# Performance work log

Measured on AMD Instinct MI355X. Metric: run time of the kernel, lower is better.

The kernel has to match this reference:

```python
import jax, jax.numpy as jnp
import numpy as np

NUM_HEADS = 16
HEAD_DIM = 80  # embed_dim 1280 / 16


def setup_inputs() -> dict:
    key = jax.random.key(0)
    ks = jax.random.split(key, 5)
    E = NUM_HEADS * HEAD_DIM
    sq, b = 1024, 8
    x = jax.random.normal(ks[0], (sq, b, E), dtype=jnp.float32)
    w_in = jax.random.normal(ks[1], (E, 3 * E), dtype=jnp.float32) * (E ** -0.5)
    b_in = jax.random.normal(ks[2], (3 * E,), dtype=jnp.float32) * 0.01
    w_out = jax.random.normal(ks[3], (E, E), dtype=jnp.float32) * (E ** -0.5)
    b_out = jax.random.normal(ks[4], (E,), dtype=jnp.float32) * 0.01
    return {"x": x, "w_in": w_in, "b_in": b_in, "w_out": w_out, "b_out": b_out}


def reference(x, w_in, b_in, w_out, b_out):
    sq, b, E = x.shape
    H, D = NUM_HEADS, HEAD_DIM
    norm_factor = jnp.asarray(D ** 0.5, x.dtype)
    # in_proj: [sq, b, 3E] -> [sq, b, H, 3D], split into q/k/v along last dim
    mixed = (x @ w_in + b_in).reshape(sq, b, H, 3 * D)
    q, k, v = jnp.split(mixed, 3, axis=-1)  # each [sq, b, H, D]
    # merge (b, H) and move to batch-of-bmm layout [b*H, sq, D]
    q = q.reshape(sq, b * H, D).transpose(1, 0, 2) / norm_factor
    k = k.reshape(sq, b * H, D).transpose(1, 0, 2)
    v = v.reshape(sq, b * H, D).transpose(1, 0, 2)
    scores = jnp.einsum('nqd,nkd->nqk', q, k)  # [b*H, sq, sq]
    probs = jax.nn.softmax(scores, axis=-1)
    ctx = jnp.einsum('nqk,nkd->nqd', probs, v)  # [b*H, sq, D]
    # [b, H, sq, D] -> [sq, b, H, D] -> [sq, b, E]
    ctx = ctx.reshape(b, H, sq, D).transpose(2, 0, 1, 3).reshape(sq, b, E)
    return ctx @ w_out + b_out
```

## Files before the change

### kernel.cpp

```cpp
#include <hip/hip_runtime.h>

#define DEVI __device__ __forceinline__

typedef _Float16 f16x8 __attribute__((ext_vector_type(8)));
typedef _Float16 f16x4v __attribute__((ext_vector_type(4)));
typedef _Float16 f16x2 __attribute__((ext_vector_type(2)));
typedef __fp16 fp16x2 __attribute__((ext_vector_type(2)));
typedef float f32x4 __attribute__((ext_vector_type(4)));
typedef float f32x16 __attribute__((ext_vector_type(16)));
typedef unsigned u32x4 __attribute__((ext_vector_type(4)));

DEVI void gl16(const void* g, void* l) {
  __builtin_amdgcn_global_load_lds((const __attribute__((address_space(1))) void*)g,
                                   (__attribute__((address_space(3))) void*)l, 16, 0, 0);
}

#define VMCNT(N) asm volatile("s_waitcnt vmcnt(" #N ")" ::: "memory")
#define LGKM0() asm volatile("s_waitcnt lgkmcnt(0)" ::: "memory")
#define BARRIER() asm volatile("s_barrier" ::: "memory")

DEVI unsigned pk2(float a, float b) {
  fp16x2 t = __builtin_amdgcn_cvt_pkrtz(a, b);
  return __builtin_bit_cast(unsigned, t);
}
DEVI void pl32swap(unsigned &a, unsigned &b) {
  asm volatile("v_permlane32_swap_b32 %0, %1" : "+v"(a), "+v"(b));
}

__global__ __launch_bounds__(256) void k_prep(const float* __restrict__ x, _Float16* __restrict__ xb,
                                              const float* __restrict__ w_in, _Float16* __restrict__ w_inT,
                                              const float* __restrict__ w_out, _Float16* __restrict__ w_outT) {
  __shared__ float t[32][33];
  int bid = blockIdx.x;
  int tid = threadIdx.x;
  if (bid < 2048) {
    const int n4 = 8192 * 1280 / 4;
    for (int i = bid * 256 + tid; i < n4; i += 2048 * 256) {
      float4 v = ((const float4*)x)[i];
      f16x4v h = { (_Float16)v.x, (_Float16)v.y, (_Float16)v.z, (_Float16)v.w };
      ((f16x4v*)xb)[i] = h;
    }
    return;
  }
  const float* in; _Float16* out; int R, C, tIdx; bool perm;
  if (bid < 6848) { in = w_in;  out = w_inT;  R = 1280; C = 3840; tIdx = bid - 2048; perm = true; }
  else            { in = w_out; out = w_outT; R = 1280; C = 1280; tIdx = bid - 6848; perm = false; }
  int ntc = C / 32;
  int cb = (tIdx % ntc) * 32, rb = (tIdx / ntc) * 32;
  int tx = tid & 31, ty = tid >> 5;
  #pragma unroll
  for (int i = ty; i < 32; i += 8) t[i][tx] = in[(size_t)(rb + i) * C + cb + tx];
  __syncthreads();
  #pragma unroll
  for (int i = ty; i < 32; i += 8) {
    int c = cb + i;
    if (perm) {
      int hq = c / 240, tt = c - hq * 240;
      int reg = tt / 80, d = tt - reg * 80;
      c = reg * 1280 + hq * 80 + d;
    }
    out[(size_t)c * R + rb + tx] = (_Float16)t[tx][i];
  }
}


#define MM(NLO, AF, BF) do {                                                                       \
    __builtin_amdgcn_s_setprio(1);                                                                 \
    _Pragma("unroll")                                                                              \
    for (int m_ = 0; m_ < 8; m_++) {                                                               \
      acc[m_][NLO]     = __builtin_amdgcn_mfma_f32_16x16x32_f16(AF[m_], BF[NLO],     acc[m_][NLO],     0, 0, 0); \
      acc[m_][NLO + 1] = __builtin_amdgcn_mfma_f32_16x16x32_f16(AF[m_], BF[NLO + 1], acc[m_][NLO + 1], 0, 0, 0); \
    }                                                                                              \
    __builtin_amdgcn_s_setprio(0);                                                                 \
  } while (0)

#define LDA(KT, KK, DST) do {                                                                      \
    const _Float16* bas_ = &smem[(size_t)((((KT) & 1) * 2) + wr) * 8192];                          \
    _Pragma("unroll")                                                                              \
    for (int m_ = 0; m_ < 8; m_++)                                                                 \
      DST[m_] = *(const f16x8*)&bas_[(m_ * 16 + ln) * 64 + (((((KK) * 4) + g) ^ chB) << 3)];       \
  } while (0)

#define LDB(KT, KK, DST) do {                                                                      \
    const _Float16* bas_ = &smem[32768 + (size_t)((((KT) & 1) * 2) + (wc >> 1)) * 8192];           \
    _Pragma("unroll")                                                                              \
    for (int n_ = 0; n_ < 4; n_++)                                                                 \
      DST[n_] = *(const f16x8*)&bas_[((wc & 1) * 64 + n_ * 16 + ln) * 64 + (((((KK) * 4) + g) ^ chB) << 3)]; \
  } while (0)

template<int M, int N, int K>
__global__ __launch_bounds__(512, 2) void k_gemm8(const _Float16* __restrict__ A, const _Float16* __restrict__ BT,
                                                  const float* __restrict__ bias,
                                                  _Float16* __restrict__ qo, _Float16* __restrict__ ko,
                                                  _Float16* __restrict__ vo) {
  extern __shared__ _Float16 smem[];
  constexpr int NT = K / 64;
  constexpr int NI = NT / 2;
  const int tid = threadIdx.x;
  const int w = tid >> 6, lane = tid & 63, ln = lane & 15, g = lane >> 4;
  const int wr = w >> 2, wc = w & 3;
  const int l8 = lane >> 3, l7 = lane & 7;
  const int stChunk = (l7 ^ l8) << 3;
  const int chB = ln & 7;

  constexpr int MT = M / 256;
  const int xcd = blockIdx.x & 7;
  const int i = blockIdx.x >> 3;
  const int bm0 = (xcd * (MT / 8) + (i & 3)) * 256;
  const int bn0 = (i >> 2) * 256;

  auto stgA = [&](int kt, int hh) {
    _Float16* ldsb = &smem[(size_t)((kt & 1) * 2 + hh) * 8192 + w * 1024];
    const _Float16* g0 = &A[(size_t)(bm0 + hh * 128 + w * 16 + l8) * K + kt * 64 + stChunk];
    gl16(g0, ldsb);
    gl16(g0 + (size_t)8 * K, ldsb + 512);
  };
  auto stgB = [&](int kt, int hh) {
    _Float16* ldsb = &smem[32768 + (size_t)((kt & 1) * 2 + hh) * 8192 + w * 1024];
    const _Float16* g0 = &BT[(size_t)(bn0 + hh * 128 + w * 16 + l8) * K + kt * 64 + stChunk];
    gl16(g0, ldsb);
    gl16(g0 + (size_t)8 * K, ldsb + 512);
  };

  f32x4 acc[8][4] = {};
  f16x8 a0[8], a1[8], b0[4], b1[4];

  stgB(0, 0); stgB(0, 1); stgA(0, 0); stgA(0, 1);
  stgB(1, 0); stgB(1, 1); stgA(1, 0);
  VMCNT(6);
  BARRIER();
  LDA(0, 0, a0); LDB(0, 0, b0);

  for (int it = 0; it < NI; ++it) {
    const int T0 = 2 * it, T1 = 2 * it + 1;
    const int S0 = (T0 + 2 < NT) ? T0 + 2 : 0;
    const int S1 = (T1 + 2 < NT) ? T1 + 2 : 1;
    LDB(T0, 1, b1);
    stgA(T1, 1);
    BARRIER();
    MM(0, a0, b0);
    LGKM0(); BARRIER();
    LDA(T0, 1, a1);
    stgB(S0, 0);
    BARRIER();
    MM(2, a0, b0);
    LGKM0(); BARRIER();
    stgB(S0, 1);
    BARRIER();
    MM(0, a1, b1);
    VMCNT(4);
    LGKM0(); BARRIER();
    LDA(T1, 0, a0); LDB(T1, 0, b0);
    stgA(S0, 0);
    BARRIER();
    MM(2, a1, b1);
    LGKM0(); BARRIER();
    LDB(T1, 1, b1);
    stgA(S0, 1);
    BARRIER();
    MM(0, a0, b0);
    LGKM0(); BARRIER();
    LDA(T1, 1, a1);
    stgB(S1, 0);
    BARRIER();
    MM(2, a0, b0);
    LGKM0(); BARRIER();
    stgB(S1, 1);
    BARRIER();
    MM(0, a1, b1);
    VMCNT(4);
    LGKM0(); BARRIER();
    LDA(S0, 0, a0); LDB(S0, 0, b0);
    stgA(S1, 0);
    BARRIER();
    MM(2, a1, b1);
    LGKM0(); BARRIER();
  }

  VMCNT(0);
  BARRIER();
  _Float16* sH = smem;
  const int regn = bn0 / 1280;
  const int relb = bn0 - regn * 1280;
  #pragma unroll
  for (int n = 0; n < 4; n++) {
    int col = wc * 64 + n * 16 + ln;
    int rel = relb + col;
    int h = rel / 80, d = rel - h * 80;
    float bv = bias[h * 240 + regn * 80 + d];
    float scl = (regn == 0) ? (0.11180339887498948f * 1.4426950408889634f) : 1.0f;
    #pragma unroll
    for (int m = 0; m < 8; m++) {
      #pragma unroll
      for (int r = 0; r < 4; r++) {
        int row = wr * 128 + m * 16 + 4 * g + r;
        sH[row * 256 + col] = (_Float16)((acc[m][n][r] + bv) * scl);
      }
    }
  }
  LGKM0();
  BARRIER();
  _Float16* dst = (regn == 0) ? qo : (regn == 1) ? ko : vo;
  #pragma unroll
  for (int i2 = 0; i2 < 16; i2++) {
    int id = tid + 512 * i2;
    int row = id >> 5, c8 = id & 31;
    f16x8 v = *(const f16x8*)&sH[row * 256 + c8 * 8];
    int rel = relb + c8 * 8;
    int h = rel / 80, d0 = rel - h * 80;
    int grow = bm0 + row;
    *(f16x8*)&dst[(size_t)(((grow & 7) * 16 + h) * 1024 + (grow >> 3)) * 80 + d0] = v;
  }
}


#define MMo(NLO, AF, BF) do {                                                                      \
    __builtin_amdgcn_s_setprio(1);                                                                 \
    _Pragma("unroll")                                                                              \
    for (int m_ = 0; m_ < 4; m_++) {                                                               \
      acc[m_][NLO]     = __builtin_amdgcn_mfma_f32_16x16x32_f16(AF[m_], BF[NLO],     acc[m_][NLO],     0, 0, 0); \
      acc[m_][NLO + 1] = __builtin_amdgcn_mfma_f32_16x16x32_f16(AF[m_], BF[NLO + 1], acc[m_][NLO + 1], 0, 0, 0); \
    }                                                                                              \
    __builtin_amdgcn_s_setprio(0);                                                                 \
  } while (0)

#define LDAo(KT, KK, DST) do {                                                                     \
    const _Float16* bas_ = &smem[(size_t)((KT) & 1) * 8192];                                       \
    _Pragma("unroll")                                                                              \
    for (int m_ = 0; m_ < 4; m_++)                                                                 \
      DST[m_] = *(const f16x8*)&bas_[(wr * 64 + m_ * 16 + ln) * 64 + (((((KK) * 4) + g) ^ chB) << 3)]; \
  } while (0)

#define LDBo(KT, KK, DST) do {                                                                     \
    const _Float16* bas_ = &smem[16384 + (size_t)(((KT) & 1) * 2 + (wc >> 1)) * 8192];             \
    _Pragma("unroll")                                                                              \
    for (int n_ = 0; n_ < 4; n_++)                                                                 \
      DST[n_] = *(const f16x8*)&bas_[((wc & 1) * 64 + n_ * 16 + ln) * 64 + (((((KK) * 4) + g) ^ chB) << 3)]; \
  } while (0)

template<int M, int N, int K>
__global__ __launch_bounds__(512, 2) void k_gemm8o(const _Float16* __restrict__ A, const _Float16* __restrict__ BT,
                                                   const float* __restrict__ bias, float* __restrict__ outF) {
  extern __shared__ _Float16 smem[];
  constexpr int NT = K / 64;
  constexpr int NI = NT / 2;
  const int tid = threadIdx.x;
  const int w = tid >> 6, lane = tid & 63, ln = lane & 15, g = lane >> 4;
  const int wr = w >> 2, wc = w & 3;
  const int l8 = lane >> 3, l7 = lane & 7;
  const int stChunk = (l7 ^ l8) << 3;
  const int chB = ln & 7;

  const int xcd = blockIdx.x & 7;
  const int i = blockIdx.x >> 3;
  const int bm0 = (xcd * 8 + (i & 7)) * 128;
  const int bn0 = (i >> 3) * 256;

  auto stgA = [&](int kt) {
    _Float16* ldsb = &smem[(size_t)(kt & 1) * 8192 + w * 1024];
    const _Float16* g0 = &A[(size_t)(bm0 + w * 16 + l8) * K + kt * 64 + stChunk];
    gl16(g0, ldsb);
    gl16(g0 + (size_t)8 * K, ldsb + 512);
  };
  auto stgB = [&](int kt, int hh) {
    _Float16* ldsb = &smem[16384 + (size_t)((kt & 1) * 2 + hh) * 8192 + w * 1024];
    const _Float16* g0 = &BT[(size_t)(bn0 + hh * 128 + w * 16 + l8) * K + kt * 64 + stChunk];
    gl16(g0, ldsb);
    gl16(g0 + (size_t)8 * K, ldsb + 512);
  };

  f32x4 acc[4][4] = {};
  f16x8 a0[4], a1[4], b0[4], b1[4];

  stgB(0, 0); stgB(0, 1); stgA(0);
  stgB(1, 0); stgB(1, 1); stgA(1);
  VMCNT(6);
  BARRIER();
  LDAo(0, 0, a0); LDBo(0, 0, b0);

  for (int it = 0; it < NI; ++it) {
    const int T0 = 2 * it, T1 = 2 * it + 1;
    const int S0 = (T0 + 2 < NT) ? T0 + 2 : 0;
    const int S1 = (T1 + 2 < NT) ? T1 + 2 : 1;
    LDBo(T0, 1, b1);
    BARRIER(); MMo(0, a0, b0); LGKM0(); BARRIER();
    LDAo(T0, 1, a1);
    stgB(S0, 0);
    BARRIER(); MMo(2, a0, b0); LGKM0(); BARRIER();
    stgB(S0, 1);
    BARRIER(); MMo(0, a1, b1); VMCNT(4); LGKM0(); BARRIER();
    LDAo(T1, 0, a0); LDBo(T1, 0, b0);
    stgA(S0);
    BARRIER(); MMo(2, a1, b1); LGKM0(); BARRIER();
    LDBo(T1, 1, b1);
    BARRIER(); MMo(0, a0, b0); LGKM0(); BARRIER();
    LDAo(T1, 1, a1);
    stgB(S1, 0);
    BARRIER(); MMo(2, a0, b0); LGKM0(); BARRIER();
    stgB(S1, 1);
    BARRIER(); MMo(0, a1, b1); VMCNT(4); LGKM0(); BARRIER();
    LDAo(S0, 0, a0); LDBo(S0, 0, b0);
    stgA(S1);
    BARRIER(); MMo(2, a1, b1); LGKM0(); BARRIER();
  }

  VMCNT(0);
  #pragma unroll
  for (int n = 0; n < 4; n++) {
    int col = bn0 + wc * 64 + n * 16 + ln;
    float bv = bias[col];
    #pragma unroll
    for (int m = 0; m < 4; m++) {
      int rbase = bm0 + wr * 64 + m * 16 + 4 * g;
      #pragma unroll
      for (int r = 0; r < 4; r++)
        outF[(size_t)(rbase + r) * N + col] = acc[m][n][r] + bv;
    }
  }
}

__global__ __launch_bounds__(512, 2) void k_attn(const _Float16* __restrict__ qb, const _Float16* __restrict__ kb,
                                                 const _Float16* __restrict__ vb, _Float16* __restrict__ ctxg) {
  extern __shared__ _Float16 smem[];
  _Float16* Kb0 = smem;
  _Float16* Kb1 = smem + 8192;
  _Float16* Vb0 = smem + 16384;
  _Float16* Vb1 = smem + 16384 + 6144;

  const int tid = threadIdx.x;
  const int w = tid >> 6, lane = tid & 63;
  const int l32 = lane & 31, h = lane >> 5;
  const int lx = l32 & 7;
  const int xcd = blockIdx.x & 7;
  const int j = blockIdx.x >> 3;
  const int head = xcd + 8 * (j & 15);
  const int s0 = (j >> 4) * 256;
  const int bb = head >> 4, h16 = head & 15;

  const int cA = tid;
  const int cB = (tid < 128) ? tid + 512 : tid;
  const int sA = cA & 63, dA = cA >> 6;
  const int sB = cB & 63, dB = cB >> 6;
  const size_t hbase = (size_t)head * 81920;
  const _Float16* kGA = kb + hbase + sA * 80 + dA * 8;
  const _Float16* kGB = kb + hbase + sB * 80 + dB * 8;
  const _Float16* vGA = vb + hbase + sA * 80 + dA * 8;
  const _Float16* vGB = vb + hbase + sB * 80 + dB * 8;
  const int kOA = sA * 128 + ((dA ^ (sA & 7)) << 3);
  const int kOB = sB * 128 + ((dB ^ (sB & 7)) << 3);

  uint4 krA, krB, vrA, vrB;
  auto issue = [&](int kt) {
    krA = *(const uint4*)(kGA + kt * 5120);
    krB = *(const uint4*)(kGB + kt * 5120);
    vrA = *(const uint4*)(vGA + kt * 5120);
    vrB = *(const uint4*)(vGB + kt * 5120);
  };
  auto stage = [&](int b) {
    _Float16* kd = b ? Kb1 : Kb0;
    _Float16* vd = b ? Vb1 : Vb0;
    *(uint4*)(kd + kOA) = krA;
    *(uint4*)(kd + kOB) = krB;
    f16x8 va = __builtin_bit_cast(f16x8, vrA);
    f16x8 vbv = __builtin_bit_cast(f16x8, vrB);
    #pragma unroll
    for (int jj = 0; jj < 8; ++jj) {
      int da = dA * 8 + jj;
      vd[da * 64 + (((sA >> 3) ^ (da & 7)) << 3) + (sA & 7)] = va[jj];
      int db = dB * 8 + jj;
      vd[db * 64 + (((sB >> 3) ^ (db & 7)) << 3) + (sB & 7)] = vbv[jj];
    }
  };

  const int qrow = s0 + w * 32 + l32;
  f16x8 qf[5];
  #pragma unroll
  for (int s = 0; s < 5; s++)
    qf[s] = *(const f16x8*)&qb[(size_t)(head * 1024 + qrow) * 80 + s * 16 + h * 8];

  f32x16 ct[3] = {};
  float m_run = -INFINITY, l_run = 0.f;

  issue(0);
  stage(0);
  LGKM0();
  BARRIER();
  issue(1);

  for (int kt = 0; kt < 16; ++kt) {
    const _Float16* kc = (kt & 1) ? Kb1 : Kb0;
    const _Float16* vc = (kt & 1) ? Vb1 : Vb0;

    f32x16 sc0 = {}, sc1 = {};
    __builtin_amdgcn_s_setprio(1);
    #pragma unroll
    for (int s = 0; s < 5; ++s) {
      f16x8 kf0 = *(const f16x8*)&kc[l32 * 128 + (((2 * s + h) ^ lx) << 3)];
      f16x8 kf1 = *(const f16x8*)&kc[(32 + l32) * 128 + (((2 * s + h) ^ lx) << 3)];
      sc0 = __builtin_amdgcn_mfma_f32_32x32x16_f16(kf0, qf[s], sc0, 0, 0, 0);
      sc1 = __builtin_amdgcn_mfma_f32_32x32x16_f16(kf1, qf[s], sc1, 0, 0, 0);
    }
    __builtin_amdgcn_s_setprio(0);

    float mx[8];
    #pragma unroll
    for (int i = 0; i < 8; ++i)
      mx[i] = fmaxf(fmaxf(sc0[i], sc0[i + 8]), fmaxf(sc1[i], sc1[i + 8]));
    #pragma unroll
    for (int i = 0; i < 4; ++i) mx[i] = fmaxf(mx[i], mx[i + 4]);
    float tm = fmaxf(fmaxf(mx[0], mx[2]), fmaxf(mx[1], mx[3]));
    tm = fmaxf(tm, __shfl_xor(tm, 32));

    if (__any(tm > m_run + 8.f)) {
      float mnew = fmaxf(m_run, tm);
      float fac = exp2f(m_run - mnew);
      #pragma unroll
      for (int dt = 0; dt < 3; ++dt)
        #pragma unroll
        for (int i = 0; i < 16; ++i) ct[dt][i] *= fac;
      l_run *= fac;
      m_run = mnew;
    }

    float p0[16], p1[16];
    #pragma unroll
    for (int i = 0; i < 16; ++i) p0[i] = exp2f(sc0[i] - m_run);
    #pragma unroll
    for (int i = 0; i < 16; ++i) p1[i] = exp2f(sc1[i] - m_run);
    float ps = 0.f;
    #pragma unroll
    for (int i = 0; i < 16; ++i) ps += p0[i] + p1[i];

    unsigned fr[4][4];
    #define PACK4(T, PP) do {                                                \
        _Pragma("unroll")                                                    \
        for (int s16 = 0; s16 < 2; ++s16) {                                  \
          unsigned u0 = pk2(PP[8 * s16 + 0], PP[8 * s16 + 1]);               \
          unsigned u1 = pk2(PP[8 * s16 + 2], PP[8 * s16 + 3]);               \
          unsigned u2 = pk2(PP[8 * s16 + 4], PP[8 * s16 + 5]);               \
          unsigned u3 = pk2(PP[8 * s16 + 6], PP[8 * s16 + 7]);               \
          pl32swap(u0, u2); pl32swap(u1, u3);                                \
          fr[2 * (T) + s16][0] = u0; fr[2 * (T) + s16][1] = u1;              \
          fr[2 * (T) + s16][2] = u2; fr[2 * (T) + s16][3] = u3;              \
        }                                                                    \
      } while (0)
    PACK4(0, p0);
    PACK4(1, p1);

    l_run += ps + __shfl_xor(ps, 32);

    __builtin_amdgcn_s_setprio(1);
    #pragma unroll
    for (int ss = 0; ss < 4; ++ss) {
      u32x4 fu = { fr[ss][0], fr[ss][1], fr[ss][2], fr[ss][3] };
      f16x8 pf = __builtin_bit_cast(f16x8, fu);
      #pragma unroll
      for (int dt = 0; dt < 3; ++dt) {
        f16x8 vf = *(const f16x8*)&vc[(dt * 32 + l32) * 64 + (((2 * ss + h) ^ lx) << 3)];
        ct[dt] = __builtin_amdgcn_mfma_f32_32x32x16_f16(vf, pf, ct[dt], 0, 0, 0);
      }
    }
    __builtin_amdgcn_s_setprio(0);

    if (kt < 15) {
      stage((kt + 1) & 1);
      LGKM0();
      BARRIER();
      if (kt < 14) issue(kt + 2);
    }
  }

  float inv = 1.f / l_run;
  int sq = s0 + w * 32 + l32;
  _Float16* outp = ctxg + (size_t)(sq * 8 + bb) * 1280 + h16 * 80 + 4 * h;
  #pragma unroll
  for (int dt = 0; dt < 3; ++dt)
    #pragma unroll
    for (int rq = 0; rq < 4; ++rq) {
      if (dt == 2 && rq >= 2) continue;
      f16x4v o = { (_Float16)(ct[dt][rq * 4 + 0] * inv), (_Float16)(ct[dt][rq * 4 + 1] * inv),
                   (_Float16)(ct[dt][rq * 4 + 2] * inv), (_Float16)(ct[dt][rq * 4 + 3] * inv) };
      *(f16x4v*)&outp[dt * 32 + rq * 8] = o;
    }
}

extern "C" void kernel_launch(void* const* d_in, const int* in_sizes, int n_in,
                              void* d_out, int out_size, void* d_ws, size_t ws_size,
                              hipStream_t stream) {
  const float* x     = (const float*)d_in[0];
  const float* w_in  = (const float*)d_in[1];
  const float* b_in  = (const float*)d_in[2];
  const float* w_out = (const float*)d_in[3];
  const float* b_out = (const float*)d_in[4];
  float* out = (float*)d_out;

  char* ws = (char*)d_ws;
  size_t off = 0;
  auto carve = [&](size_t bytes) -> void* {
    void* p = ws + off;
    off += (bytes + 255) & ~(size_t)255;
    return p;
  };
  _Float16* xb     = (_Float16*)carve(8192ull * 1280 * 2);
  _Float16* w_inT  = (_Float16*)carve(3840ull * 1280 * 2);
  _Float16* w_outT = (_Float16*)carve(1280ull * 1280 * 2);
  _Float16* qb     = (_Float16*)carve(128ull * 1024 * 80 * 2);
  _Float16* kbuf   = (_Float16*)carve(128ull * 1024 * 80 * 2);
  _Float16* vbuf   = (_Float16*)carve(128ull * 1024 * 80 * 2);
  _Float16* ctxg   = (_Float16*)carve(8192ull * 1280 * 2);
  if (off > ws_size) return;

  hipFuncSetAttribute(reinterpret_cast<const void*>(&k_gemm8<8192, 3840, 1280>),
                      hipFuncAttributeMaxDynamicSharedMemorySize, 131072);
  hipFuncSetAttribute(reinterpret_cast<const void*>(&k_gemm8o<8192, 1280, 1280>),
                      hipFuncAttributeMaxDynamicSharedMemorySize, 98304);
  hipFuncSetAttribute(reinterpret_cast<const void*>(&k_attn),
                      hipFuncAttributeMaxDynamicSharedMemorySize, 57344);

  k_prep<<<8448, 256, 0, stream>>>(x, xb, w_in, w_inT, w_out, w_outT);

  k_gemm8<8192, 3840, 1280><<<480, 512, 131072, stream>>>(xb, w_inT, b_in, qb, kbuf, vbuf);
  k_attn<<<512, 512, 57344, stream>>>(qb, kbuf, vbuf, ctxg);
  k_gemm8o<8192, 1280, 1280><<<320, 512, 98304, stream>>>(ctxg, w_outT, b_out, out);
}
```

Baseline: 245.5 us.

## Fold softmax row-sum into PV MFMA via ones column and restage V transpose

The V tile is padded with a constant column of ones in the unused 80..95 rows of the third output MFMA tile. The softmax denominator then accumulates inside the PV matrix multiply instead of through a scalar sum and cross-lane shuffle every iteration. The V shared-memory staging is also rewritten: 160 threads each load four rows and pack pairs into 64-bit stores, replacing scattered 16-bit LDS writes. The row sum now carries fp16-rounded probabilities, so the normalisation differs slightly from summing in fp32.

New measurement: 244.1 us. About the same (-0.6%).

```diff
diff --git a/kernel.cpp b/kernel.cpp
--- a/kernel.cpp
+++ b/kernel.cpp
@@ -336,39 +336,57 @@
   const int head = xcd + 8 * (j & 15);
   const int s0 = (j >> 4) * 256;
   const int bb = head >> 4, h16 = head & 15;
+  const size_t hbase = (size_t)head * 81920;
 
   const int cA = tid;
   const int cB = (tid < 128) ? tid + 512 : tid;
   const int sA = cA & 63, dA = cA >> 6;
   const int sB = cB & 63, dB = cB >> 6;
-  const size_t hbase = (size_t)head * 81920;
   const _Float16* kGA = kb + hbase + sA * 80 + dA * 8;
   const _Float16* kGB = kb + hbase + sB * 80 + dB * 8;
-  const _Float16* vGA = vb + hbase + sA * 80 + dA * 8;
-  const _Float16* vGB = vb + hbase + sB * 80 + dB * 8;
   const int kOA = sA * 128 + ((dA ^ (sA & 7)) << 3);
   const int kOB = sB * 128 + ((dB ^ (sB & 7)) << 3);
 
-  uint4 krA, krB, vrA, vrB;
+  const int s4 = tid & 15, dc = tid >> 4;
+  const _Float16* vG = vb + hbase + (s4 * 4) * 80 + dc * 8;
+
+  uint4 krA, krB, vq0, vq1, vq2, vq3;
   auto issue = [&](int kt) {
     krA = *(const uint4*)(kGA + kt * 5120);
     krB = *(const uint4*)(kGB + kt * 5120);
-    vrA = *(const uint4*)(vGA + kt * 5120);
-    vrB = *(const uint4*)(vGB + kt * 5120);
+    if (tid < 160) {
+      const _Float16* p = vG + kt * 5120;
+      vq0 = *(const uint4*)(p);
+      vq1 = *(const uint4*)(p + 80);
+      vq2 = *(const uint4*)(p + 160);
+      vq3 = *(const uint4*)(p + 240);
+    }
   };
   auto stage = [&](int b) {
     _Float16* kd = b ? Kb1 : Kb0;
     _Float16* vd = b ? Vb1 : Vb0;
     *(uint4*)(kd + kOA) = krA;
     *(uint4*)(kd + kOB) = krB;
-    f16x8 va = __builtin_bit_cast(f16x8, vrA);
-    f16x8 vbv = __builtin_bit_cast(f16x8, vrB);
-    #pragma unroll
-    for (int jj = 0; jj < 8; ++jj) {
-      int da = dA * 8 + jj;
-      vd[da * 64 + (((sA >> 3) ^ (da & 7)) << 3) + (sA & 7)] = va[jj];
-      int db = dB * 8 + jj;
-      vd[db * 64 + (((sB >> 3) ^ (db & 7)) << 3) + (sB & 7)] = vbv[jj];
+    if (tid < 160) {
+      const unsigned* w0 = (const unsigned*)&vq0;
+      const unsigned* w1 = (const unsigned*)&vq1;
+      const unsigned* w2 = (const unsigned*)&vq2;
+      const unsigned* w3 = (const unsigned*)&vq3;
+      #pragma unroll
+      for (int jj = 0; jj < 8; ++jj) {
+        int jw = jj >> 1;
+        unsigned lo, hi;
+        if (jj & 1) {
+          lo = (w0[jw] >> 16) | (w1[jw] & 0xffff0000u);
+          hi = (w2[jw] >> 16) | (w3[jw] & 0xffff0000u);
+        } else {
+          lo = (w0[jw] & 0xffffu) | (w1[jw] << 16);
+          hi = (w2[jw] & 0xffffu) | (w3[jw] << 16);
+        }
+        unsigned long long u = (unsigned long long)lo | ((unsigned long long)hi << 32);
+        int d = dc * 8 + jj;
+        *(unsigned long long*)(vd + d * 64 + (((s4 >> 1) ^ jj) << 3) + ((s4 & 1) << 2)) = u;
+      }
     }
   };
 
@@ -379,10 +397,14 @@
     qf[s] = *(const f16x8*)&qb[(size_t)(head * 1024 + qrow) * 80 + s * 16 + h * 8];
 
   f32x16 ct[3] = {};
-  float m_run = -INFINITY, l_run = 0.f;
+  float m_run = -INFINITY;
 
   issue(0);
   stage(0);
+  if (tid < 64) {
+    Vb0[80 * 64 + tid] = (_Float16)1.0f;
+    Vb1[80 * 64 + tid] = (_Float16)1.0f;
+  }
   LGKM0();
   BARRIER();
   issue(1);
@@ -418,7 +440,6 @@
       for (int dt = 0; dt < 3; ++dt)
         #pragma unroll
         for (int i = 0; i < 16; ++i) ct[dt][i] *= fac;
-      l_run *= fac;
       m_run = mnew;
     }
 
@@ -427,9 +448,6 @@
     for (int i = 0; i < 16; ++i) p0[i] = exp2f(sc0[i] - m_run);
     #pragma unroll
     for (int i = 0; i < 16; ++i) p1[i] = exp2f(sc1[i] - m_run);
-    float ps = 0.f;
-    #pragma unroll
-    for (int i = 0; i < 16; ++i) ps += p0[i] + p1[i];
 
     unsigned fr[4][4];
     #define PACK4(T, PP) do {                                                \
@@ -447,8 +465,6 @@
     PACK4(0, p0);
     PACK4(1, p1);
 
-    l_run += ps + __shfl_xor(ps, 32);
-
     __builtin_amdgcn_s_setprio(1);
     #pragma unroll
     for (int ss = 0; ss < 4; ++ss) {
@@ -470,7 +486,8 @@
     }
   }
 
-  float inv = 1.f / l_run;
+  float lsum = __shfl(ct[2][8], l32);
+  float inv = 1.f / lsum;
   int sq = s0 + w * 32 + l32;
   _Float16* outp = ctxg + (size_t)(sq * 8 + bb) * 1280 + h16 * 80 + 4 * h;
   #pragma unroll
```
